# Kernel tuning notes

Measured on AMD Instinct MI355X. Metric: run time of the kernel, lower is better.

Reference implementation:

```python
import jax, jax.numpy as jnp
import numpy as np
import math

D_MODEL = 512
N_HEADS = 8
BMIN, BMAX = 0.3, 1.0
W_E, W_M, W_I = 0.4, 0.4, 0.2


def norm_minmax(t):
    t_min = t.min(axis=-1, keepdims=True)
    t_max = t.max(axis=-1, keepdims=True)
    return (t - t_min) / jnp.maximum(t_max - t_min, 1e-8)


def setup_inputs() -> dict:
    key = jax.random.key(0)
    ks = jax.random.split(key, 12)
    B, S, D, C = 2, 2048, D_MODEL, 1000
    x = jax.random.normal(ks[0], (B, S, D), dtype=jnp.float32)
    out_probs = jax.nn.softmax(jax.random.normal(ks[1], (B, C), dtype=jnp.float32), axis=-1)
    idf_seq = jax.random.uniform(ks[2], (B, S), dtype=jnp.float32)
    def lin(kw, kb):
        W = jax.random.normal(kw, (D, D), dtype=jnp.float32) * 0.02
        b = jax.random.normal(kb, (D,), dtype=jnp.float32) * 0.02
        return W, b
    Wq, bq = lin(ks[3], ks[4])
    Wk, bk = lin(ks[5], ks[6])
    Wv, bv = lin(ks[7], ks[8])
    Wo, bo = lin(ks[9], ks[10])
    return dict(x=x, out_probs=out_probs, idf_seq=idf_seq,
                Wq=Wq, bq=bq, Wk=Wk, bk=bk, Wv=Wv, bv=bv, Wo=Wo, bo=bo)


def reference(x, out_probs, idf_seq, Wq, bq, Wk, bk, Wv, bv, Wo, bo):
    B, S, D = x.shape
    H = N_HEADS
    dk = D // H

    def heads(W, b):
        # (B,S,D) -> (B,H,S,dk)
        return (x @ W.T + b).reshape(B, S, H, dk).swapaxes(1, 2)

    q = heads(Wq, bq)
    k = heads(Wk, bk)
    v = heads(Wv, bv)

    logits = jnp.einsum('bhqd,bhkd->bhqk', q, k) / math.sqrt(dk)
    attn_probs = jax.nn.softmax(logits, axis=-1)  # (B,H,S,S)

    # --- compute_load ---
    p = jnp.maximum(attn_probs, 1e-12)
    H_i = (-(p * jnp.log(p)).sum(axis=-1)).mean(axis=1)  # (B,S)
    H_i = norm_minmax(H_i)

    top2 = jax.lax.top_k(out_probs, 2)[0]  # (B,2)
    margin = jnp.maximum(top2[:, 0] - top2[:, 1], 0.0)[:, None]  # (B,1)
    margin = jnp.broadcast_to(margin, (B, S))
    margin = norm_minmax(margin)
    load_from_margin = 1.0 - margin

    L = W_E * H_i + W_M * load_from_margin + W_I * idf_seq
    L = norm_minmax(L)

    # --- map load to budget and cap ---
    Bgt = BMIN + (BMAX - BMIN) * L  # (B,S)
    row_sum = jnp.maximum(attn_probs.sum(axis=-1, keepdims=True), 1e-12)  # (B,H,S,1)
    scale = jnp.minimum(Bgt[:, None, :, None] / row_sum, 1.0)
    attn_probs = attn_probs * scale

    y = jnp.einsum('bhqk,bhkd->bhqd', attn_probs, v)  # (B,H,S,dk)
    y = y.swapaxes(1, 2).reshape(B, S, D)
    y = y @ Wo.T + bo
    return y, attn_probs
```

## Files before the change

### kernel.cpp

```cpp
#include <hip/hip_runtime.h>
#include <hip/hip_bf16.h>


typedef __attribute__((ext_vector_type(8))) short bf16x8;
typedef __attribute__((ext_vector_type(4))) float f32x4;

static __device__ __forceinline__ unsigned short f2b(float f) {
  union { float f; unsigned int u; } v; v.f = f;
  unsigned int u = v.u;
  u += 0x7FFF + ((u >> 16) & 1);
  return (unsigned short)(u >> 16);
}

static __device__ __forceinline__ void lds_barrier() {
  asm volatile("s_waitcnt lgkmcnt(0)\n\ts_barrier" ::: "memory");
}

__global__ __launch_bounds__(256) void cvt_all(
    const float* __restrict__ x,
    const float* __restrict__ Wq, const float* __restrict__ Wk,
    const float* __restrict__ Wv, const float* __restrict__ Wo,
    unsigned short* __restrict__ xb, unsigned short* __restrict__ wqkv,
    unsigned short* __restrict__ wob)
{
  int i = blockIdx.x * 256 + threadIdx.x;
  const float* s; unsigned short* d; int off;
  if (i < 524288) { s = x; d = xb; off = i; }
  else {
    int j = i - 524288; int w = j >> 16; off = j & 65535;
    switch (w) {
      case 0: s = Wq; d = wqkv; break;
      case 1: s = Wk; d = wqkv + 262144; break;
      case 2: s = Wv; d = wqkv + 524288; break;
      default: s = Wo; d = wob; break;
    }
  }
  float4 v = reinterpret_cast<const float4*>(s)[off];
  ushort4 o;
  o.x = f2b(v.x); o.y = f2b(v.y); o.z = f2b(v.z); o.w = f2b(v.w);
  reinterpret_cast<ushort4*>(d)[off] = o;
}

__global__ __launch_bounds__(256) void qkv_gemm(
    const unsigned short* __restrict__ xb, const unsigned short* __restrict__ w,
    const float* __restrict__ bq, const float* __restrict__ bk, const float* __restrict__ bv,
    unsigned short* __restrict__ Qb, unsigned short* __restrict__ Kb,
    unsigned short* __restrict__ Vtb)
{
  __shared__ unsigned short smem[5120];
  unsigned short* shA = smem;
  unsigned short* shB = smem + 2560;
  const int tid = threadIdx.x;
  const int bm = blockIdx.x, bn = blockIdx.y;
  const int lane = tid & 63, wid = tid >> 6;
  const int wr = wid >> 1, wc = wid & 1;
  const int lg = lane >> 4, lc = lane & 15;

  f32x4 acc[2][2];
#pragma unroll
  for (int i = 0; i < 2; ++i)
#pragma unroll
    for (int j = 0; j < 2; ++j) acc[i][j] = f32x4{0.f, 0.f, 0.f, 0.f};

  const int row_st = tid >> 2;
  const int k8 = (tid & 3) * 8;
  for (int kt = 0; kt < 16; ++kt) {
    *reinterpret_cast<uint4*>(&shA[row_st * 40 + k8]) =
        *reinterpret_cast<const uint4*>(&xb[(size_t)(bm * 64 + row_st) * 512 + kt * 32 + k8]);
    *reinterpret_cast<uint4*>(&shB[row_st * 40 + k8]) =
        *reinterpret_cast<const uint4*>(&w[(size_t)(bn * 64 + row_st) * 512 + kt * 32 + k8]);
    __syncthreads();
    bf16x8 af[2], bfr[2];
#pragma unroll
    for (int f = 0; f < 2; ++f) {
      af[f]  = *reinterpret_cast<const bf16x8*>(&shA[(wr * 32 + f * 16 + lc) * 40 + lg * 8]);
      bfr[f] = *reinterpret_cast<const bf16x8*>(&shB[(wc * 32 + f * 16 + lc) * 40 + lg * 8]);
    }
#pragma unroll
    for (int fm = 0; fm < 2; ++fm)
#pragma unroll
      for (int fn = 0; fn < 2; ++fn)
        acc[fm][fn] = __builtin_amdgcn_mfma_f32_16x16x32_bf16(af[fm], bfr[fn], acc[fm][fn], 0, 0, 0);
    __syncthreads();
  }

  if (bn < 16) {
#pragma unroll
    for (int fm = 0; fm < 2; ++fm)
#pragma unroll
      for (int fn = 0; fn < 2; ++fn)
#pragma unroll
        for (int r = 0; r < 4; ++r) {
          int mi = bm * 64 + wr * 32 + fm * 16 + lg * 4 + r;
          int ni = bn * 64 + wc * 32 + fn * 16 + lc;
          int bb = mi >> 11, s = mi & 2047;
          float v = acc[fm][fn][r];
          if (ni < 512) {
            int h = ni >> 6, d = ni & 63;
            v = (v + bq[ni]) * 0.125f;
            Qb[(((size_t)bb * 8 + h) * 2048 + s) * 64 + d] = f2b(v);
          } else {
            int i2 = ni - 512; int h = i2 >> 6, d = i2 & 63;
            v += bk[i2];
            Kb[(((size_t)bb * 8 + h) * 2048 + s) * 64 + d] = f2b(v);
          }
        }
  } else {
    unsigned short (*T)[80] = reinterpret_cast<unsigned short(*)[80]>(smem);
    __syncthreads();
#pragma unroll
    for (int fm = 0; fm < 2; ++fm)
#pragma unroll
      for (int fn = 0; fn < 2; ++fn)
#pragma unroll
        for (int r = 0; r < 4; ++r) {
          int nl = wc * 32 + fn * 16 + lc;
          int ml = wr * 32 + fm * 16 + lg * 4 + r;
          int i2 = (bn - 16) * 64 + nl;
          T[nl][ml] = f2b(acc[fm][fn][r] + bv[i2]);
        }
    __syncthreads();
    const int row = tid >> 3;
    const int seg = tid & 7;
    const int h = bn - 16;
    int mi = bm * 64 + seg * 8;
    int bb = mi >> 11, s = mi & 2047;
#pragma unroll
    for (int rr = 0; rr < 2; ++rr) {
      int d = row + rr * 32;
      *reinterpret_cast<uint4*>(&Vtb[(((size_t)bb * 8 + h) * 64 + d) * 2048 + s]) =
          *reinterpret_cast<const uint4*>(&T[d][seg * 8]);
    }
  }
}

__global__ __launch_bounds__(256) void attn_pass1(
    const unsigned short* __restrict__ Qb, const unsigned short* __restrict__ Kb,
    float* __restrict__ zA, float* __restrict__ tA)
{
  __shared__ unsigned short Kbuf[2][4096];
  const int l = blockIdx.x;
  const int l2 = (l & 7) * 64 + (l >> 3);
  const int bh = l2 >> 5;
  const int qt = l2 & 31;
  const int tid = threadIdx.x;
  const int lane = tid & 63, wid = tid >> 6;
  const int lg = lane >> 4, lc = lane & 15;
  const int q0 = qt * 64 + wid * 16;
  const unsigned short* Qp = Qb + (size_t)bh * 2048 * 64;
  const unsigned short* Kp = Kb + (size_t)bh * 2048 * 64;
  bf16x8 aq0 = *reinterpret_cast<const bf16x8*>(&Qp[(q0 + lc) * 64 + lg * 8]);
  bf16x8 aq1 = *reinterpret_cast<const bf16x8*>(&Qp[(q0 + lc) * 64 + lg * 8 + 32]);

  const int srow = tid >> 3;
  const int sseg = tid & 7;
  const int wIdx0 = (srow * 64 + sseg * 8) ^ ((srow & 7) << 3);
  const int wIdx1 = wIdx0 + 2048;
  const int rswz = (lc & 7) << 3;

  float Z_ = 0.f, T_ = 0.f;

  {
    uint4 g0 = *reinterpret_cast<const uint4*>(&Kp[(size_t)srow * 64 + sseg * 8]);
    uint4 g1 = *reinterpret_cast<const uint4*>(&Kp[(size_t)(srow + 32) * 64 + sseg * 8]);
    *reinterpret_cast<uint4*>(&Kbuf[0][wIdx0]) = g0;
    *reinterpret_cast<uint4*>(&Kbuf[0][wIdx1]) = g1;
    lds_barrier();
  }

  for (int t = 0; t < 32; ++t) {
    uint4 g0, g1;
    if (t < 31) {
      g0 = *reinterpret_cast<const uint4*>(&Kp[(size_t)((t + 1) * 64 + srow) * 64 + sseg * 8]);
      g1 = *reinterpret_cast<const uint4*>(&Kp[(size_t)((t + 1) * 64 + srow + 32) * 64 + sseg * 8]);
    }
    const unsigned short* kb = Kbuf[t & 1];
    f32x4 acc[4];
#pragma unroll
    for (int c = 0; c < 4; ++c) {
      int rI = (c * 16 + lc) * 64;
      bf16x8 b0 = *reinterpret_cast<const bf16x8*>(&kb[(rI + lg * 8) ^ rswz]);
      bf16x8 b1 = *reinterpret_cast<const bf16x8*>(&kb[(rI + 32 + lg * 8) ^ rswz]);
      f32x4 z = {0.f, 0.f, 0.f, 0.f};
      z = __builtin_amdgcn_mfma_f32_16x16x32_bf16(b0, aq0, z, 0, 0, 0);
      acc[c] = __builtin_amdgcn_mfma_f32_16x16x32_bf16(b1, aq1, z, 0, 0, 0);
    }
#pragma unroll
    for (int c = 0; c < 4; ++c) {
#pragma unroll
      for (int r = 0; r < 4; ++r) {
        float lv = acc[c][r];
        float e = __expf(lv);
        Z_ += e;
        T_ = fmaf(lv, e, T_);
      }
    }
    if (t < 31) {
      *reinterpret_cast<uint4*>(&Kbuf[(t + 1) & 1][wIdx0]) = g0;
      *reinterpret_cast<uint4*>(&Kbuf[(t + 1) & 1][wIdx1]) = g1;
    }
    lds_barrier();
  }
  Z_ += __shfl_xor(Z_, 16); T_ += __shfl_xor(T_, 16);
  Z_ += __shfl_xor(Z_, 32); T_ += __shfl_xor(T_, 32);
  if (lane < 16) {
    int idx = bh * 2048 + q0 + lc;
    zA[idx] = Z_; tA[idx] = T_;
  }
}

__global__ __launch_bounds__(256) void load_kernel(
    const float* __restrict__ zA, const float* __restrict__ tA,
    const float* __restrict__ idf, float* __restrict__ scaleArr)
{
  const int b = blockIdx.x, t = threadIdx.x;
  __shared__ float sh[2048];
  __shared__ float rmin[256], rmax[256];
  for (int s = t; s < 2048; s += 256) {
    float acc = 0.f;
    for (int h = 0; h < 8; ++h) {
      int idx = (b * 8 + h) * 2048 + s;
      float Z = zA[idx];
      acc += logf(Z) - tA[idx] / Z;
    }
    sh[s] = acc * 0.125f;
  }
  __syncthreads();
  float mn = 3e38f, mx = -3e38f;
  for (int s = t; s < 2048; s += 256) { float v = sh[s]; mn = fminf(mn, v); mx = fmaxf(mx, v); }
  rmin[t] = mn; rmax[t] = mx; __syncthreads();
  for (int o = 128; o > 0; o >>= 1) {
    if (t < o) { rmin[t] = fminf(rmin[t], rmin[t + o]); rmax[t] = fmaxf(rmax[t], rmax[t + o]); }
    __syncthreads();
  }
  float Hmin = rmin[0], Hmax = rmax[0];
  __syncthreads();
  for (int s = t; s < 2048; s += 256) {
    float Hn = (sh[s] - Hmin) / fmaxf(Hmax - Hmin, 1e-8f);
    sh[s] = 0.4f * Hn + 0.4f + 0.2f * idf[b * 2048 + s];
  }
  __syncthreads();
  mn = 3e38f; mx = -3e38f;
  for (int s = t; s < 2048; s += 256) { float v = sh[s]; mn = fminf(mn, v); mx = fmaxf(mx, v); }
  rmin[t] = mn; rmax[t] = mx; __syncthreads();
  for (int o = 128; o > 0; o >>= 1) {
    if (t < o) { rmin[t] = fminf(rmin[t], rmin[t + o]); rmax[t] = fmaxf(rmax[t], rmax[t + o]); }
    __syncthreads();
  }
  float Lmin = rmin[0], Lmax = rmax[0];
  for (int s = t; s < 2048; s += 256) {
    float Ln = (sh[s] - Lmin) / fmaxf(Lmax - Lmin, 1e-8f);
    scaleArr[b * 2048 + s] = fminf(0.3f + 0.7f * Ln, 1.0f);
  }
}

__global__ __launch_bounds__(256) void attn_pass2(
    const unsigned short* __restrict__ Qb, const unsigned short* __restrict__ Kb,
    const unsigned short* __restrict__ Vtb,
    const float* __restrict__ zA, const float* __restrict__ scaleArr,
    float* __restrict__ attnOut, unsigned short* __restrict__ yh)
{
  __shared__ unsigned short Kbuf[2][4096];
  __shared__ unsigned short Vbuf[2][4096];
  __shared__ unsigned short Pb[4][16 * 72];
  const int l = blockIdx.x;
  const int l2 = (l & 7) * 64 + (l >> 3);
  const int bh = l2 >> 5;
  const int qt = l2 & 31;
  const int b = bh >> 3; const int h = bh & 7;
  const int tid = threadIdx.x;
  const int lane = tid & 63, wid = tid >> 6;
  const int lg = lane >> 4, lc = lane & 15;
  const int q0 = qt * 64 + wid * 16;
  const unsigned short* Qp = Qb + (size_t)bh * 2048 * 64;
  const unsigned short* Kp = Kb + (size_t)bh * 2048 * 64;
  const unsigned short* Vp = Vtb + (size_t)bh * 64 * 2048;
  bf16x8 aq0 = *reinterpret_cast<const bf16x8*>(&Qp[(q0 + lc) * 64 + lg * 8]);
  bf16x8 aq1 = *reinterpret_cast<const bf16x8*>(&Qp[(q0 + lc) * 64 + lg * 8 + 32]);
  const float coefL = scaleArr[b * 2048 + q0 + lc] / zA[bh * 2048 + q0 + lc];
  f32x4 accY[4];
#pragma unroll
  for (int i = 0; i < 4; ++i) accY[i] = f32x4{0.f, 0.f, 0.f, 0.f};
  unsigned short* myP = Pb[wid];
  float* aBase = attnOut + (size_t)bh * 2048 * 2048;

  const int srow = tid >> 3, sseg = tid & 7;
  const int wIdx0 = (srow * 64 + sseg * 8) ^ ((srow & 7) << 3);
  const int wIdx1 = wIdx0 + 2048;
  const int rswz = (lc & 7) << 3;

  {
    uint4 k0_ = *reinterpret_cast<const uint4*>(&Kp[(size_t)srow * 64 + sseg * 8]);
    uint4 k1_ = *reinterpret_cast<const uint4*>(&Kp[(size_t)(srow + 32) * 64 + sseg * 8]);
    uint4 v0_ = *reinterpret_cast<const uint4*>(&Vp[(size_t)srow * 2048 + sseg * 8]);
    uint4 v1_ = *reinterpret_cast<const uint4*>(&Vp[(size_t)(srow + 32) * 2048 + sseg * 8]);
    *reinterpret_cast<uint4*>(&Kbuf[0][wIdx0]) = k0_;
    *reinterpret_cast<uint4*>(&Kbuf[0][wIdx1]) = k1_;
    *reinterpret_cast<uint4*>(&Vbuf[0][wIdx0]) = v0_;
    *reinterpret_cast<uint4*>(&Vbuf[0][wIdx1]) = v1_;
    lds_barrier();
  }

  for (int t = 0; t < 32; ++t) {
    uint4 gk0, gk1, gv0, gv1;
    if (t < 31) {
      int kn = (t + 1) * 64;
      gk0 = *reinterpret_cast<const uint4*>(&Kp[(size_t)(kn + srow) * 64 + sseg * 8]);
      gk1 = *reinterpret_cast<const uint4*>(&Kp[(size_t)(kn + srow + 32) * 64 + sseg * 8]);
      gv0 = *reinterpret_cast<const uint4*>(&Vp[(size_t)srow * 2048 + kn + sseg * 8]);
      gv1 = *reinterpret_cast<const uint4*>(&Vp[(size_t)(srow + 32) * 2048 + kn + sseg * 8]);
    }
    const unsigned short* kb = Kbuf[t & 1];
    const unsigned short* vb = Vbuf[t & 1];
    f32x4 acc[4];
#pragma unroll
    for (int c = 0; c < 4; ++c) {
      int rI = (c * 16 + lc) * 64;
      bf16x8 b0 = *reinterpret_cast<const bf16x8*>(&kb[(rI + lg * 8) ^ rswz]);
      bf16x8 b1 = *reinterpret_cast<const bf16x8*>(&kb[(rI + 32 + lg * 8) ^ rswz]);
      f32x4 z = {0.f, 0.f, 0.f, 0.f};
      z = __builtin_amdgcn_mfma_f32_16x16x32_bf16(b0, aq0, z, 0, 0, 0);
      acc[c] = __builtin_amdgcn_mfma_f32_16x16x32_bf16(b1, aq1, z, 0, 0, 0);
    }
#pragma unroll
    for (int c = 0; c < 4; ++c) {
      ushort4 pw;
      pw.x = f2b(__expf(acc[c][0]) * coefL);
      pw.y = f2b(__expf(acc[c][1]) * coefL);
      pw.z = f2b(__expf(acc[c][2]) * coefL);
      pw.w = f2b(__expf(acc[c][3]) * coefL);
      *reinterpret_cast<ushort4*>(&myP[lc * 72 + c * 16 + lg * 4]) = pw;
    }
    const int k0g = t * 64;
#pragma unroll
    for (int j = 0; j < 4; ++j) {
      int row = j * 4 + lg;
      ushort4 p4 = *reinterpret_cast<const ushort4*>(&myP[row * 72 + lc * 4]);
      f32x4 v;
      v[0] = __uint_as_float((unsigned)p4.x << 16);
      v[1] = __uint_as_float((unsigned)p4.y << 16);
      v[2] = __uint_as_float((unsigned)p4.z << 16);
      v[3] = __uint_as_float((unsigned)p4.w << 16);
      *reinterpret_cast<f32x4*>(&aBase[(size_t)(q0 + row) * 2048 + k0g + lc * 4]) = v;
    }
#pragma unroll
    for (int kk = 0; kk < 2; ++kk) {
      bf16x8 ap = *reinterpret_cast<const bf16x8*>(&myP[lc * 72 + kk * 32 + lg * 8]);
#pragma unroll
      for (int cf = 0; cf < 4; ++cf) {
        int rI = (cf * 16 + lc) * 64;
        bf16x8 bv_ = *reinterpret_cast<const bf16x8*>(&vb[(rI + kk * 32 + lg * 8) ^ rswz]);
        accY[cf] = __builtin_amdgcn_mfma_f32_16x16x32_bf16(ap, bv_, accY[cf], 0, 0, 0);
      }
    }
    if (t < 31) {
      *reinterpret_cast<uint4*>(&Kbuf[(t + 1) & 1][wIdx0]) = gk0;
      *reinterpret_cast<uint4*>(&Kbuf[(t + 1) & 1][wIdx1]) = gk1;
      *reinterpret_cast<uint4*>(&Vbuf[(t + 1) & 1][wIdx0]) = gv0;
      *reinterpret_cast<uint4*>(&Vbuf[(t + 1) & 1][wIdx1]) = gv1;
    }
    lds_barrier();
  }
#pragma unroll
  for (int cf = 0; cf < 4; ++cf)
#pragma unroll
    for (int r = 0; r < 4; ++r) {
      int qrow = q0 + lg * 4 + r;
      yh[((size_t)b * 2048 + qrow) * 512 + h * 64 + cf * 16 + lc] = f2b(accY[cf][r]);
    }
}

__global__ __launch_bounds__(256) void out_gemm(
    const unsigned short* __restrict__ yhb, const unsigned short* __restrict__ wo,
    const float* __restrict__ bo, float* __restrict__ yOut)
{
  __shared__ unsigned short shA[64 * 40];
  __shared__ unsigned short shB[64 * 40];
  const int tid = threadIdx.x;
  const int bm = blockIdx.x, bn = blockIdx.y;
  const int lane = tid & 63, wid = tid >> 6;
  const int wr = wid >> 1, wc = wid & 1;
  const int lg = lane >> 4, lc = lane & 15;

  f32x4 acc[2][2];
#pragma unroll
  for (int i = 0; i < 2; ++i)
#pragma unroll
    for (int j = 0; j < 2; ++j) acc[i][j] = f32x4{0.f, 0.f, 0.f, 0.f};

  const int row_st = tid >> 2;
  const int k8 = (tid & 3) * 8;
  for (int kt = 0; kt < 16; ++kt) {
    *reinterpret_cast<uint4*>(&shA[row_st * 40 + k8]) =
        *reinterpret_cast<const uint4*>(&yhb[(size_t)(bm * 64 + row_st) * 512 + kt * 32 + k8]);
    *reinterpret_cast<uint4*>(&shB[row_st * 40 + k8]) =
        *reinterpret_cast<const uint4*>(&wo[(size_t)(bn * 64 + row_st) * 512 + kt * 32 + k8]);
    __syncthreads();
    bf16x8 af[2], bfr[2];
#pragma unroll
    for (int f = 0; f < 2; ++f) {
      af[f]  = *reinterpret_cast<const bf16x8*>(&shA[(wr * 32 + f * 16 + lc) * 40 + lg * 8]);
      bfr[f] = *reinterpret_cast<const bf16x8*>(&shB[(wc * 32 + f * 16 + lc) * 40 + lg * 8]);
    }
#pragma unroll
    for (int fm = 0; fm < 2; ++fm)
#pragma unroll
      for (int fn = 0; fn < 2; ++fn)
        acc[fm][fn] = __builtin_amdgcn_mfma_f32_16x16x32_bf16(af[fm], bfr[fn], acc[fm][fn], 0, 0, 0);
    __syncthreads();
  }
#pragma unroll
  for (int fm = 0; fm < 2; ++fm)
#pragma unroll
    for (int fn = 0; fn < 2; ++fn)
#pragma unroll
      for (int r = 0; r < 4; ++r) {
        int mi = bm * 64 + wr * 32 + fm * 16 + lg * 4 + r;
        int ni = bn * 64 + wc * 32 + fn * 16 + lc;
        yOut[(size_t)mi * 512 + ni] = acc[fm][fn][r] + bo[ni];
      }
}

extern "C" void kernel_launch(void* const* d_in, const int* in_sizes, int n_in,
                              void* d_out, int out_size, void* d_ws, size_t ws_size,
                              hipStream_t stream) {
  const float* x   = (const float*)d_in[0];
  const float* idf = (const float*)d_in[2];
  const float* Wq = (const float*)d_in[3];
  const float* bq = (const float*)d_in[4];
  const float* Wk = (const float*)d_in[5];
  const float* bk = (const float*)d_in[6];
  const float* Wv = (const float*)d_in[7];
  const float* bv = (const float*)d_in[8];
  const float* Wo = (const float*)d_in[9];
  const float* bo = (const float*)d_in[10];

  float* yOut = (float*)d_out;
  float* attnOut = yOut + (size_t)2 * 2048 * 512;

  char* p = (char*)d_ws;
  auto alloc = [&](size_t bytes) { char* r = p; p += (bytes + 255) & ~(size_t)255; return r; };
  unsigned short* xb   = (unsigned short*)alloc((size_t)2097152 * 2);
  unsigned short* wqkv = (unsigned short*)alloc((size_t)786432 * 2);
  unsigned short* wob  = (unsigned short*)alloc((size_t)262144 * 2);
  unsigned short* Qb   = (unsigned short*)alloc((size_t)2097152 * 2);
  unsigned short* Kb   = (unsigned short*)alloc((size_t)2097152 * 2);
  unsigned short* Vtb  = (unsigned short*)alloc((size_t)2097152 * 2);
  unsigned short* yh   = (unsigned short*)alloc((size_t)2097152 * 2);
  float* zA = (float*)alloc((size_t)32768 * 4);
  float* tA = (float*)alloc((size_t)32768 * 4);
  float* scaleArr = (float*)alloc((size_t)4096 * 4);

  cvt_all<<<3072, 256, 0, stream>>>(x, Wq, Wk, Wv, Wo, xb, wqkv, wob);
  qkv_gemm<<<dim3(64, 24), 256, 0, stream>>>(xb, wqkv, bq, bk, bv, Qb, Kb, Vtb);
  attn_pass1<<<512, 256, 0, stream>>>(Qb, Kb, zA, tA);
  load_kernel<<<2, 256, 0, stream>>>(zA, tA, idf, scaleArr);
  attn_pass2<<<512, 256, 0, stream>>>(Qb, Kb, Vtb, zA, scaleArr, attnOut, yh);
  out_gemm<<<dim3(64, 8), 256, 0, stream>>>(yh, wob, bo, yOut);
}
```

Before: 124.2 us.

## Enlarge QKV GEMM tiles to 128x128 and reuse P fragments for attn stores

Result: slower. 147.7 us (+19.0%).

```diff
diff --git a/kernel.cpp b/kernel.cpp
--- a/kernel.cpp
+++ b/kernel.cpp
@@ -47,52 +47,58 @@
     unsigned short* __restrict__ Qb, unsigned short* __restrict__ Kb,
     unsigned short* __restrict__ Vtb)
 {
-  __shared__ unsigned short smem[5120];
+  __shared__ unsigned short smem[10240];
   unsigned short* shA = smem;
-  unsigned short* shB = smem + 2560;
+  unsigned short* shB = smem + 5120;
   const int tid = threadIdx.x;
   const int bm = blockIdx.x, bn = blockIdx.y;
   const int lane = tid & 63, wid = tid >> 6;
   const int wr = wid >> 1, wc = wid & 1;
   const int lg = lane >> 4, lc = lane & 15;
 
-  f32x4 acc[2][2];
-#pragma unroll
-  for (int i = 0; i < 2; ++i)
-#pragma unroll
-    for (int j = 0; j < 2; ++j) acc[i][j] = f32x4{0.f, 0.f, 0.f, 0.f};
-
-  const int row_st = tid >> 2;
-  const int k8 = (tid & 3) * 8;
+  f32x4 acc[4][4];
+#pragma unroll
+  for (int i = 0; i < 4; ++i)
+#pragma unroll
+    for (int j = 0; j < 4; ++j) acc[i][j] = f32x4{0.f, 0.f, 0.f, 0.f};
+
+  const int row_st = tid >> 1;
+  const int kh16 = (tid & 1) * 16;
   for (int kt = 0; kt < 16; ++kt) {
-    *reinterpret_cast<uint4*>(&shA[row_st * 40 + k8]) =
-        *reinterpret_cast<const uint4*>(&xb[(size_t)(bm * 64 + row_st) * 512 + kt * 32 + k8]);
-    *reinterpret_cast<uint4*>(&shB[row_st * 40 + k8]) =
-        *reinterpret_cast<const uint4*>(&w[(size_t)(bn * 64 + row_st) * 512 + kt * 32 + k8]);
-    __syncthreads();
-    bf16x8 af[2], bfr[2];
-#pragma unroll
-    for (int f = 0; f < 2; ++f) {
-      af[f]  = *reinterpret_cast<const bf16x8*>(&shA[(wr * 32 + f * 16 + lc) * 40 + lg * 8]);
-      bfr[f] = *reinterpret_cast<const bf16x8*>(&shB[(wc * 32 + f * 16 + lc) * 40 + lg * 8]);
-    }
-#pragma unroll
-    for (int fm = 0; fm < 2; ++fm)
-#pragma unroll
-      for (int fn = 0; fn < 2; ++fn)
+    const size_t aOff = (size_t)(bm * 128 + row_st) * 512 + kt * 32 + kh16;
+    const size_t bOff = (size_t)(bn * 128 + row_st) * 512 + kt * 32 + kh16;
+    *reinterpret_cast<uint4*>(&shA[row_st * 40 + kh16]) =
+        *reinterpret_cast<const uint4*>(&xb[aOff]);
+    *reinterpret_cast<uint4*>(&shA[row_st * 40 + kh16 + 8]) =
+        *reinterpret_cast<const uint4*>(&xb[aOff + 8]);
+    *reinterpret_cast<uint4*>(&shB[row_st * 40 + kh16]) =
+        *reinterpret_cast<const uint4*>(&w[bOff]);
+    *reinterpret_cast<uint4*>(&shB[row_st * 40 + kh16 + 8]) =
+        *reinterpret_cast<const uint4*>(&w[bOff + 8]);
+    __syncthreads();
+    bf16x8 af[4], bfr[4];
+#pragma unroll
+    for (int f = 0; f < 4; ++f) {
+      af[f]  = *reinterpret_cast<const bf16x8*>(&shA[(wr * 64 + f * 16 + lc) * 40 + lg * 8]);
+      bfr[f] = *reinterpret_cast<const bf16x8*>(&shB[(wc * 64 + f * 16 + lc) * 40 + lg * 8]);
+    }
+#pragma unroll
+    for (int fm = 0; fm < 4; ++fm)
+#pragma unroll
+      for (int fn = 0; fn < 4; ++fn)
         acc[fm][fn] = __builtin_amdgcn_mfma_f32_16x16x32_bf16(af[fm], bfr[fn], acc[fm][fn], 0, 0, 0);
     __syncthreads();
   }
 
-  if (bn < 16) {
-#pragma unroll
-    for (int fm = 0; fm < 2; ++fm)
-#pragma unroll
-      for (int fn = 0; fn < 2; ++fn)
+  if (bn < 8) {
+#pragma unroll
+    for (int fm = 0; fm < 4; ++fm)
+#pragma unroll
+      for (int fn = 0; fn < 4; ++fn)
 #pragma unroll
         for (int r = 0; r < 4; ++r) {
-          int mi = bm * 64 + wr * 32 + fm * 16 + lg * 4 + r;
-          int ni = bn * 64 + wc * 32 + fn * 16 + lc;
+          int mi = bm * 128 + wr * 64 + fm * 16 + lg * 4 + r;
+          int ni = bn * 128 + wc * 64 + fn * 16 + lc;
           int bb = mi >> 11, s = mi & 2047;
           float v = acc[fm][fn][r];
           if (ni < 512) {
@@ -106,30 +112,34 @@
           }
         }
   } else {
-    unsigned short (*T)[80] = reinterpret_cast<unsigned short(*)[80]>(smem);
-    __syncthreads();
-#pragma unroll
-    for (int fm = 0; fm < 2; ++fm)
-#pragma unroll
-      for (int fn = 0; fn < 2; ++fn)
-#pragma unroll
-        for (int r = 0; r < 4; ++r) {
-          int nl = wc * 32 + fn * 16 + lc;
-          int ml = wr * 32 + fm * 16 + lg * 4 + r;
-          int i2 = (bn - 16) * 64 + nl;
-          T[nl][ml] = f2b(acc[fm][fn][r] + bv[i2]);
-        }
-    __syncthreads();
-    const int row = tid >> 3;
-    const int seg = tid & 7;
-    const int h = bn - 16;
-    int mi = bm * 64 + seg * 8;
-    int bb = mi >> 11, s = mi & 2047;
-#pragma unroll
-    for (int rr = 0; rr < 2; ++rr) {
-      int d = row + rr * 32;
-      *reinterpret_cast<uint4*>(&Vtb[(((size_t)bb * 8 + h) * 64 + d) * 2048 + s]) =
-          *reinterpret_cast<const uint4*>(&T[d][seg * 8]);
+    unsigned short (*T)[136] = reinterpret_cast<unsigned short(*)[136]>(smem);
+    const int bb = bm >> 4;
+    const int s0 = (bm & 15) * 128;
+#pragma unroll
+    for (int half = 0; half < 2; ++half) {
+      __syncthreads();
+      if (wc == half) {
+#pragma unroll
+        for (int fm = 0; fm < 4; ++fm)
+#pragma unroll
+          for (int fn = 0; fn < 4; ++fn)
+#pragma unroll
+            for (int r = 0; r < 4; ++r) {
+              int dl = fn * 16 + lc;
+              int sl = wr * 64 + fm * 16 + lg * 4 + r;
+              int i2 = (bn - 8) * 128 + half * 64 + dl;
+              T[dl][sl] = f2b(acc[fm][fn][r] + bv[i2]);
+            }
+      }
+      __syncthreads();
+      const int d = tid >> 2;
+      const int ss = (tid & 3) * 32;
+      const int h = (bn - 8) * 2 + half;
+      unsigned short* vdst = &Vtb[(((size_t)bb * 8 + h) * 64 + d) * 2048 + s0 + ss];
+#pragma unroll
+      for (int j = 0; j < 4; ++j)
+        *reinterpret_cast<uint4*>(vdst + j * 8) =
+            *reinterpret_cast<const uint4*>(&T[d][ss + j * 8]);
     }
   }
 }
@@ -333,19 +343,17 @@
     }
     const int k0g = t * 64;
 #pragma unroll
-    for (int j = 0; j < 4; ++j) {
-      int row = j * 4 + lg;
-      ushort4 p4 = *reinterpret_cast<const ushort4*>(&myP[row * 72 + lc * 4]);
-      f32x4 v;
-      v[0] = __uint_as_float((unsigned)p4.x << 16);
-      v[1] = __uint_as_float((unsigned)p4.y << 16);
-      v[2] = __uint_as_float((unsigned)p4.z << 16);
-      v[3] = __uint_as_float((unsigned)p4.w << 16);
-      *reinterpret_cast<f32x4*>(&aBase[(size_t)(q0 + row) * 2048 + k0g + lc * 4]) = v;
-    }
-#pragma unroll
     for (int kk = 0; kk < 2; ++kk) {
       bf16x8 ap = *reinterpret_cast<const bf16x8*>(&myP[lc * 72 + kk * 32 + lg * 8]);
+      f32x4 v0, v1;
+#pragma unroll
+      for (int j = 0; j < 4; ++j) {
+        v0[j] = __uint_as_float((unsigned)(unsigned short)ap[j] << 16);
+        v1[j] = __uint_as_float((unsigned)(unsigned short)ap[j + 4] << 16);
+      }
+      float* dst = &aBase[(size_t)(q0 + lc) * 2048 + k0g + kk * 32 + lg * 8];
+      *reinterpret_cast<f32x4*>(dst) = v0;
+      *reinterpret_cast<f32x4*>(dst + 4) = v1;
 #pragma unroll
       for (int cf = 0; cf < 4; ++cf) {
         int rI = (cf * 16 + lc) * 64;
@@ -452,7 +460,7 @@
   float* scaleArr = (float*)alloc((size_t)4096 * 4);
 
   cvt_all<<<3072, 256, 0, stream>>>(x, Wq, Wk, Wv, Wo, xb, wqkv, wob);
-  qkv_gemm<<<dim3(64, 24), 256, 0, stream>>>(xb, wqkv, bq, bk, bv, Qb, Kb, Vtb);
+  qkv_gemm<<<dim3(32, 12), 256, 0, stream>>>(xb, wqkv, bq, bk, bv, Qb, Kb, Vtb);
   attn_pass1<<<512, 256, 0, stream>>>(Qb, Kb, zA, tA);
   load_kernel<<<2, 256, 0, stream>>>(zA, tA, idf, scaleArr);
   attn_pass2<<<512, 256, 0, stream>>>(Qb, Kb, Vtb, zA, scaleArr, attnOut, yh);
```
